# Kernel tuning notes

Hardware: AMD Instinct MI355X
Metric: run time of the kernel (lower is better)

Reference implementation:

```python
import jax, jax.numpy as jnp
import numpy as np

N, H, E, K = 256, 128, 64, 4  # nodes, hidden, dist-embed dim, heads
ALPHA = 0.2  # leaky-relu slope


def setup_inputs() -> dict:
    key = jax.random.key(0)
    ks = jax.random.split(key, 12)
    s = lambda k, sh: (jax.random.normal(k, sh, jnp.float32) * 0.05)
    return dict(
        action_hidden_state=jax.random.normal(ks[0], (N, H), jnp.float32),
        goal_hidden_state=jax.random.normal(ks[1], (N, H), jnp.float32),
        goal=jax.random.normal(ks[2], (N, 2), jnp.float32),
        action=jax.random.normal(ks[3], (N, 2), jnp.float32),
        W_emb=s(ks[4], (1, E)), b_emb=jnp.zeros((E,), jnp.float32),
        W_gate=s(ks[5], (2 * E + 2 * H, H)), b_gate=jnp.zeros((H,), jnp.float32),
        W_gat=s(ks[6], (K, H, H)), a_src=s(ks[7], (K, H)), a_dst=s(ks[8], (K, H)),
        gat_bias=jnp.zeros((H,), jnp.float32),
    )


def cal_dist(goal, action):
    # Vectorized, math-faithful (incl. source typos) version of the O(n^2) loop.
    ax, ay = action[:, 0], action[:, 1]
    gx, gy = goal[:, 0], goal[:, 1]
    a1x, a1y = ax[:, None], ay[:, None]   # node i
    a2x, a2y = ax[None, :], ay[None, :]   # node j
    g1x, g1y = gx[:, None], gy[:, None]
    g2x, g2y = gx[None, :], gy[None, :]
    dn = (a1x - a1x) * (g1y - g2y) - (a1y - a2y) * (g1x - g2x)
    cross_a = a1x * a2y - a1y * a2x
    gterm = g1x * g2y - g1x * g2x
    n1 = cross_a * (g1x - g2x) - (a1x - a2x) * gterm
    n2 = cross_a * (g1y - g2y) - (a1y - a2x) * gterm
    safe = jnp.where(dn == 0.0, 1.0, dn)
    p1, p2 = n1 / safe, n2 / safe
    base = jnp.linalg.norm(action - goal, axis=-1)  # [n]
    d1p = jnp.sqrt((a1x - p1) ** 2 + (a1y - p2) ** 2)
    d2p = jnp.sqrt((a2x - p1) ** 2 + (a2y - p2) ** 2)
    cond = (dn != 0.0) & ((a1x - p1) * (p1 - g1x) > 0.0)
    ones = jnp.ones_like(dn)
    d1 = jnp.where(cond, d1p, base[:, None] * ones)
    d2 = jnp.where(cond, d2p, base[None, :] * ones)
    n = d1.shape[0]
    ii = jnp.arange(n)[:, None]
    jj = jnp.arange(n)[None, :]
    # dist[i,j]=d1(i,j) for i<j; dist[j,i]=d2(i,j) i.e. lower triangle = d2.T; diag = |a_i - g_i|
    return jnp.where(ii == jj, base[:, None] * ones, jnp.where(ii < jj, d1, d2.T))


def reference(action_hidden_state, goal_hidden_state, goal, action,
              W_emb, b_emb, W_gate, b_gate, W_gat, a_src, a_dst, gat_bias):
    ha, hg = action_hidden_state, goal_hidden_state
    n, h = ha.shape
    dist = cal_dist(goal, action)                      # [n,n]
    emb = dist[..., None] * W_emb[0] + b_emb           # Linear(1,E) -> [n,n,E]
    # pairwise interaction gate (i != idx branch, computed for all pairs)
    gate_in = jnp.concatenate([
        jnp.broadcast_to(ha[:, None, :], (n, n, h)),
        jnp.broadcast_to(ha[None, :, :], (n, n, h)),
        emb, jnp.swapaxes(emb, 0, 1)], axis=-1)        # [n,n,2H+2E]
    gate = jax.nn.sigmoid(gate_in @ W_gate + b_gate)   # [n,n,H]
    gated = ha[None, :, :] * gate
    # self branch: gates the goal hidden state; action row stays ungated
    emb_d = emb[jnp.arange(n), jnp.arange(n)]          # [n,E]
    gate_self = jax.nn.sigmoid(
        jnp.concatenate([ha, hg, emb_d, emb_d], axis=-1) @ W_gate + b_gate)
    curr_goal = hg * gate_self                         # [n,H]
    eye = jnp.eye(n, dtype=bool)[..., None]
    curr_action = jnp.where(eye, ha[:, None, :], gated)          # [n,n,H]
    gat_in = jnp.concatenate([curr_action, curr_goal[:, None, :]], axis=1)  # [n,n+1,H]
    # multi-head GAT layer (batched over the n query nodes)
    hp = jnp.einsum('bmf,kfo->bkmo', gat_in, W_gat)    # [n,K,m,H]
    attn = (jnp.einsum('bkmo,ko->bkm', hp, a_src)[..., :, None]
            + jnp.einsum('bkmo,ko->bkm', hp, a_dst)[..., None, :])  # [n,K,m,m]
    attn = jax.nn.softmax(jax.nn.leaky_relu(attn, ALPHA), axis=-1)
    out = jnp.einsum('bkij,bkjo->bkio', attn, hp).mean(axis=1) + gat_bias  # [n,m,H]
    out = jax.nn.elu(out)
    idx = jnp.arange(n)
    return out[idx, idx]                               # [n,H]
```

## Files before the change

kernel.cpp:

```cpp
#include <hip/hip_runtime.h>
#include <math.h>

#define N 256
#define H 128
#define E 64
#define K 4
#define M (N + 1)
#define WAVES 16
#define BLOCK 1024

__device__ __forceinline__ float sigm(float x) {
    return __fdividef(1.0f, 1.0f + __expf(-x));
}

__device__ __forceinline__ float wave_sum(float v) {
#pragma unroll
    for (int d = 1; d < 64; d <<= 1) v += __shfl_xor(v, d, 64);
    return v;
}

__device__ __forceinline__ float readlane_f(float v, int l) {
    return __uint_as_float(__builtin_amdgcn_readlane(__float_as_uint(v), l));
}

__device__ __forceinline__ float kbutterfly(float q0, float q1, float q2, float q3,
                                            int lane) {
    const bool b1 = lane & 1;
    const bool b2 = lane & 2;
    float aA = b1 ? q1 : q0, aB = b1 ? q0 : q1;
    aA += __shfl_xor(aB, 1, 64);
    float cA = b1 ? q3 : q2, cB = b1 ? q2 : q3;
    cA += __shfl_xor(cB, 1, 64);
    float eA = b2 ? cA : aA, eB = b2 ? aA : cA;
    eA += __shfl_xor(eB, 2, 64);
#pragma unroll
    for (int d = 4; d < 64; d <<= 1) eA += __shfl_xor(eA, d, 64);
    return eA;
}

__device__ __forceinline__ void pairdist(
    float a1x, float a1y, float a2x, float a2y,
    float g1x, float g1y, float g2x, float g2y,
    float baseR, float baseC, float& d_rc, float& d_cr)
{
    float t  = __fmul_rn(__fsub_rn(a1y, a2y), __fsub_rn(g1x, g2x));
    float dn = -t;
    float ca = __fsub_rn(__fmul_rn(a1x, a2y), __fmul_rn(a1y, a2x));
    float gt = __fsub_rn(__fmul_rn(g1x, g2y), __fmul_rn(g1x, g2x));
    float n1 = __fsub_rn(__fmul_rn(ca, __fsub_rn(g1x, g2x)),
                         __fmul_rn(__fsub_rn(a1x, a2x), gt));
    float n2 = __fsub_rn(__fmul_rn(ca, __fsub_rn(g1y, g2y)),
                         __fmul_rn(__fsub_rn(a1y, a2x), gt));
    float safe = (dn == 0.0f) ? 1.0f : dn;
    float p1 = __fdiv_rn(n1, safe);
    float p2 = __fdiv_rn(n2, safe);
    bool cond = (dn != 0.0f) &&
                (__fmul_rn(__fsub_rn(a1x, p1), __fsub_rn(p1, g1x)) > 0.0f);
    float dx1 = __fsub_rn(a1x, p1), dy1 = __fsub_rn(a1y, p2);
    float d1p = __fsqrt_rn(__fadd_rn(__fmul_rn(dx1, dx1), __fmul_rn(dy1, dy1)));
    float dx2 = __fsub_rn(a2x, p1), dy2 = __fsub_rn(a2y, p2);
    float d2p = __fsqrt_rn(__fadd_rn(__fmul_rn(dx2, dx2), __fmul_rn(dy2, dy2)));
    d_rc = cond ? d1p : baseR;
    d_cr = cond ? d2p : baseC;
}

__global__ __launch_bounds__(BLOCK) void gat_pre(
    const float* __restrict__ ha, const float* __restrict__ hg,
    const float* __restrict__ W_emb, const float* __restrict__ b_emb,
    const float* __restrict__ W_gate, const float* __restrict__ b_gate,
    const float* __restrict__ W_gat, const float* __restrict__ a_src,
    const float* __restrict__ a_dst,
    float* __restrict__ A1, float* __restrict__ A2, float* __restrict__ G2,
    float* __restrict__ u3g, float* __restrict__ u4g, float* __restrict__ ccg,
    float* __restrict__ vsrc, float* __restrict__ vdst)
{
    const int b    = blockIdx.x;
    const int tid  = threadIdx.x;
    const int wid  = tid >> 6;
    const int lane = tid & 63;

    __shared__ float sRed[8][3][H];

    {
        const int f  = tid & (H - 1);
        const int sl = tid >> 7;
        const int g0 = sl * 16;
        float s1 = 0.f, s2 = 0.f, s3 = 0.f;
#pragma unroll
        for (int g = 0; g < 16; ++g) {
            const int gg = g0 + g;
            float w1 = W_gate[gg * H + f];
            float w2 = W_gate[(H + gg) * H + f];
            float av = ha[b * H + gg];
            float gv = hg[b * H + gg];
            s1 += av * w1;
            s2 += av * w2;
            s3 += gv * w2;
        }
        sRed[sl][0][f] = s1;
        sRed[sl][1][f] = s2;
        sRed[sl][2][f] = s3;
    }
    __syncthreads();
    if (tid < H) {
        float r1 = 0.f, r2 = 0.f, r3 = 0.f;
#pragma unroll
        for (int sl = 0; sl < 8; ++sl) {
            r1 += sRed[sl][0][tid];
            r2 += sRed[sl][1][tid];
            r3 += sRed[sl][2][tid];
        }
        A1[b * H + tid] = r1;
        A2[b * H + tid] = r2;
        G2[b * H + tid] = r3;
    }

    if (b < 8) {
        const int k = b >> 1;
        const float2 as = *(const float2*)&a_src[k * H + lane * 2];
        const float2 ad = *(const float2*)&a_dst[k * H + lane * 2];
#pragma unroll
        for (int it = 0; it < 4; ++it) {
            const int pair = b * 64 + wid * 4 + it;
            const int f    = pair & (H - 1);
            const float2 w = *(const float2*)&W_gat[(k * H + f) * H + lane * 2];
            float vs = wave_sum(w.x * as.x + w.y * as.y);
            float vv = wave_sum(w.x * ad.x + w.y * ad.y);
            if (lane == 0) { vsrc[k * H + f] = vs; vdst[k * H + f] = vv; }
        }
    } else if (b == 8) {
        __syncthreads();
        const int f  = tid & (H - 1);
        const int sl = tid >> 7;
        float s3 = 0.f, s4 = 0.f, scc = 0.f;
#pragma unroll
        for (int e0 = 0; e0 < 8; ++e0) {
            const int e = sl * 8 + e0;
            float w3 = W_gate[(2 * H + e) * H + f];
            float w4 = W_gate[(2 * H + E + e) * H + f];
            float we = W_emb[e], be = b_emb[e];
            s3  += we * w3;
            s4  += we * w4;
            scc += be * (w3 + w4);
        }
        sRed[sl][0][f] = s3;
        sRed[sl][1][f] = s4;
        sRed[sl][2][f] = scc;
        __syncthreads();
        if (tid < H) {
            float r3 = 0.f, r4 = 0.f, rc = 0.f;
#pragma unroll
            for (int sl = 0; sl < 8; ++sl) {
                r3 += sRed[sl][0][tid];
                r4 += sRed[sl][1][tid];
                rc += sRed[sl][2][tid];
            }
            u3g[tid] = r3;
            u4g[tid] = r4;
            ccg[tid] = rc + b_gate[tid];
        }
    }
}

__global__ __launch_bounds__(BLOCK) void gat_main(
    const float* __restrict__ ha, const float* __restrict__ hg,
    const float* __restrict__ W_gat, const float* __restrict__ gat_bias,
    const float* __restrict__ A1, const float* __restrict__ A2,
    const float* __restrict__ G2,
    const float* __restrict__ u3a, const float* __restrict__ u4a,
    const float* __restrict__ cca,
    const float* __restrict__ vsrc, const float* __restrict__ vdst,
    const float* __restrict__ goal, const float* __restrict__ action,
    float* __restrict__ out)
{
    const int i    = blockIdx.x;
    const int tid  = threadIdx.x;
    const int wid  = tid >> 6;
    const int lane = tid & 63;
    const int f0   = lane * 2;

    __shared__ float2 sAct[N];
    __shared__ float2 sGoal[N];
    __shared__ float  sBase[N];
    __shared__ float2 sD[M];
    __shared__ float  sW[WAVES][K][H];
    __shared__ float  sL[WAVES][K];
    __shared__ float  sWfin[K][H];
    __shared__ float  sPart[8][H];

    const float2 a1v = *(const float2*)&A1[i * H + f0];
    const float2 haI = *(const float2*)&ha[i * H + f0];
    const float2 hgI = *(const float2*)&hg[i * H + f0];
    const float2 g2v = *(const float2*)&G2[i * H + f0];
    const float2 u3  = *(const float2*)&u3a[f0];
    const float2 u4  = *(const float2*)&u4a[f0];
    const float2 cc  = *(const float2*)&cca[f0];
    const float2 vd0 = *(const float2*)&vdst[0 * H + f0];
    const float2 vd1 = *(const float2*)&vdst[1 * H + f0];
    const float2 vd2 = *(const float2*)&vdst[2 * H + f0];
    const float2 vd3 = *(const float2*)&vdst[3 * H + f0];
    const float2 vs0 = *(const float2*)&vsrc[0 * H + f0];
    const float2 vs1 = *(const float2*)&vsrc[1 * H + f0];
    const float2 vs2 = *(const float2*)&vsrc[2 * H + f0];
    const float2 vs3 = *(const float2*)&vsrc[3 * H + f0];

    for (int t = tid; t < N; t += BLOCK) {
        float2 a = ((const float2*)action)[t];
        float2 g = ((const float2*)goal)[t];
        sAct[t]  = a;
        sGoal[t] = g;
        float dx = __fsub_rn(a.x, g.x), dy = __fsub_rn(a.y, g.y);
        sBase[t] = __fsqrt_rn(__fadd_rn(__fmul_rn(dx, dx), __fmul_rn(dy, dy)));
    }
    __syncthreads();

    if (tid < M) {
        const int j = tid;
        float dij = 0.f, dji = 0.f;
        if (j != i && j != N) {
            const float2 aI = sAct[i], gI = sGoal[i];
            const float2 aJ = sAct[j], gJ = sGoal[j];
            if (i < j)
                pairdist(aI.x, aI.y, aJ.x, aJ.y, gI.x, gI.y, gJ.x, gJ.y,
                         sBase[i], sBase[j], dij, dji);
            else
                pairdist(aJ.x, aJ.y, aI.x, aI.y, gJ.x, gJ.y, gI.x, gI.y,
                         sBase[j], sBase[i], dji, dij);
        }
        sD[j] = make_float2(dij, dji);
    }

    const float scOwn = kbutterfly(haI.x * vs0.x + haI.y * vs0.y,
                                   haI.x * vs1.x + haI.y * vs1.y,
                                   haI.x * vs2.x + haI.y * vs2.y,
                                   haI.x * vs3.x + haI.y * vs3.y, lane);

    const float2 a1cc = make_float2(a1v.x + cc.x, a1v.y + cc.y);
    const float baseI = sBase[i];
    __syncthreads();

    float l_ = 0.f;
    float w00 = 0.f, w01 = 0.f, w02 = 0.f, w03 = 0.f;
    float w10 = 0.f, w11 = 0.f, w12 = 0.f, w13 = 0.f;

#pragma unroll
    for (int t = 0; t < 16; ++t) {
        const int jj = wid + 16 * t;
        const float2 a2 = *(const float2*)&A2[jj * H + f0];
        const float2 hj = *(const float2*)&ha[jj * H + f0];
        const float2 d  = sD[jj];
        float tx = a1cc.x + a2.x + d.x * u3.x + d.y * u4.x;
        float ty = a1cc.y + a2.y + d.x * u3.y + d.y * u4.y;
        float2 g = make_float2(hj.x * sigm(tx), hj.y * sigm(ty));
        if (jj == i) g = haI;

        float q0 = g.x * vd0.x + g.y * vd0.y;
        float q1 = g.x * vd1.x + g.y * vd1.y;
        float q2 = g.x * vd2.x + g.y * vd2.y;
        float q3 = g.x * vd3.x + g.y * vd3.y;
        float e  = kbutterfly(q0, q1, q2, q3, lane);

        float lg = scOwn + e;
        lg = (lg >= 0.f) ? lg : 0.2f * lg;
        const float p = __expf(lg);
        l_ += p;

        const float p0 = readlane_f(p, 0), p1 = readlane_f(p, 1);
        const float p2 = readlane_f(p, 2), p3 = readlane_f(p, 3);
        w00 += p0 * g.x;  w10 += p0 * g.y;
        w01 += p1 * g.x;  w11 += p1 * g.y;
        w02 += p2 * g.x;  w12 += p2 * g.y;
        w03 += p3 * g.x;  w13 += p3 * g.y;
    }

    if (wid == 0) {
        float tx = a1cc.x + g2v.x + baseI * (u3.x + u4.x);
        float ty = a1cc.y + g2v.y + baseI * (u3.y + u4.y);
        float2 g = make_float2(hgI.x * sigm(tx), hgI.y * sigm(ty));

        float q0 = g.x * vd0.x + g.y * vd0.y;
        float q1 = g.x * vd1.x + g.y * vd1.y;
        float q2 = g.x * vd2.x + g.y * vd2.y;
        float q3 = g.x * vd3.x + g.y * vd3.y;
        float e  = kbutterfly(q0, q1, q2, q3, lane);

        float lg = scOwn + e;
        lg = (lg >= 0.f) ? lg : 0.2f * lg;
        const float p = __expf(lg);
        l_ += p;

        const float p0 = readlane_f(p, 0), p1 = readlane_f(p, 1);
        const float p2 = readlane_f(p, 2), p3 = readlane_f(p, 3);
        w00 += p0 * g.x;  w10 += p0 * g.y;
        w01 += p1 * g.x;  w11 += p1 * g.y;
        w02 += p2 * g.x;  w12 += p2 * g.y;
        w03 += p3 * g.x;  w13 += p3 * g.y;
    }

    *(float2*)&sW[wid][0][f0] = make_float2(w00, w10);
    *(float2*)&sW[wid][1][f0] = make_float2(w01, w11);
    *(float2*)&sW[wid][2][f0] = make_float2(w02, w12);
    *(float2*)&sW[wid][3][f0] = make_float2(w03, w13);
    if (lane < K) sL[wid][lane] = l_;
    __syncthreads();

    if (tid < K * H) {
        const int k = tid >> 7;
        const int f = tid & (H - 1);
        float W = 0.f;
#pragma unroll
        for (int w = 0; w < WAVES; ++w) W += sW[w][k][f];
        float L = 0.f;
#pragma unroll
        for (int w = 0; w < WAVES; ++w) L += sL[w][k];
        sWfin[k][f] = W / L;
    }
    __syncthreads();

    {
        const int f = tid & (H - 1);
        const int s = tid >> 7;
        float acc = 0.0f;
#pragma unroll
        for (int k = 0; k < K; ++k) {
            const int g0 = s * 16;
#pragma unroll
            for (int g = 0; g < 16; ++g)
                acc += sWfin[k][g0 + g] * W_gat[(k * H + g0 + g) * H + f];
        }
        sPart[s][f] = acc;
    }
    __syncthreads();

    if (tid < H) {
        float acc = 0.0f;
#pragma unroll
        for (int s = 0; s < 8; ++s) acc += sPart[s][tid];
        float val = 0.25f * acc + gat_bias[tid];
        out[i * H + tid] = (val > 0.0f) ? val : expm1f(val);
    }
}

extern "C" void kernel_launch(void* const* d_in, const int* in_sizes, int n_in,
                              void* d_out, int out_size, void* d_ws, size_t ws_size,
                              hipStream_t stream)
{
    const float* ha       = (const float*)d_in[0];
    const float* hg       = (const float*)d_in[1];
    const float* goal     = (const float*)d_in[2];
    const float* action   = (const float*)d_in[3];
    const float* W_emb    = (const float*)d_in[4];
    const float* b_emb    = (const float*)d_in[5];
    const float* W_gate   = (const float*)d_in[6];
    const float* b_gate   = (const float*)d_in[7];
    const float* W_gat    = (const float*)d_in[8];
    const float* a_src    = (const float*)d_in[9];
    const float* a_dst    = (const float*)d_in[10];
    const float* gat_bias = (const float*)d_in[11];

    float* ws  = (float*)d_ws;
    float* A1  = ws;
    float* A2  = A1 + N * H;
    float* G2  = A2 + N * H;
    float* u3  = G2 + N * H;
    float* u4  = u3 + H;
    float* cc  = u4 + H;
    float* vs  = cc + H;
    float* vd  = vs + K * H;

    hipLaunchKernelGGL(gat_pre, dim3(N), dim3(BLOCK), 0, stream,
                       ha, hg, W_emb, b_emb, W_gate, b_gate,
                       W_gat, a_src, a_dst,
                       A1, A2, G2, u3, u4, cc, vs, vd);

    hipLaunchKernelGGL(gat_main, dim3(N), dim3(BLOCK), 0, stream,
                       ha, hg, W_gat, gat_bias,
                       A1, A2, G2, u3, u4, cc, vs, vd,
                       goal, action, (float*)d_out);
}
```

Baseline: 28.47 us.

## Pack A2 and ha into float4 rows and spread pre-kernel side work across blocks

The pre-kernel now writes A2 interleaved with the action hidden state as one float4 array, so the main loop issues a single 16-byte load per neighbour instead of two 8-byte loads. The vsrc/vdst projections are spread across all 256 blocks, two waves each, and the u3/u4/cc reduction is split over two blocks instead of being serialized in blocks 0-8. This removes the tail imbalance in the pre-kernel and halves the load instruction count in the hot loop. The cost is an extra shared-memory stage and an extra barrier in the pre-kernel.

```diff
diff --git a/kernel.cpp b/kernel.cpp
--- a/kernel.cpp
+++ b/kernel.cpp
@@ -70,9 +70,10 @@
     const float* __restrict__ W_gate, const float* __restrict__ b_gate,
     const float* __restrict__ W_gat, const float* __restrict__ a_src,
     const float* __restrict__ a_dst,
-    float* __restrict__ A1, float* __restrict__ A2, float* __restrict__ G2,
+    float* __restrict__ A1, float* __restrict__ G2,
     float* __restrict__ u3g, float* __restrict__ u4g, float* __restrict__ ccg,
-    float* __restrict__ vsrc, float* __restrict__ vdst)
+    float* __restrict__ vsrc, float* __restrict__ vdst,
+    float4* __restrict__ pk)
 {
     const int b    = blockIdx.x;
     const int tid  = threadIdx.x;
@@ -80,6 +81,8 @@
     const int lane = tid & 63;
 
     __shared__ float sRed[8][3][H];
+    __shared__ float sA2[H];
+    __shared__ float sU[8][3][64];
 
     {
         const int f  = tid & (H - 1);
@@ -101,37 +104,22 @@
         sRed[sl][1][f] = s2;
         sRed[sl][2][f] = s3;
     }
-    __syncthreads();
-    if (tid < H) {
-        float r1 = 0.f, r2 = 0.f, r3 = 0.f;
-#pragma unroll
-        for (int sl = 0; sl < 8; ++sl) {
-            r1 += sRed[sl][0][tid];
-            r2 += sRed[sl][1][tid];
-            r3 += sRed[sl][2][tid];
-        }
-        A1[b * H + tid] = r1;
-        A2[b * H + tid] = r2;
-        G2[b * H + tid] = r3;
-    }
-
-    if (b < 8) {
-        const int k = b >> 1;
-        const float2 as = *(const float2*)&a_src[k * H + lane * 2];
-        const float2 ad = *(const float2*)&a_dst[k * H + lane * 2];
-#pragma unroll
-        for (int it = 0; it < 4; ++it) {
-            const int pair = b * 64 + wid * 4 + it;
-            const int f    = pair & (H - 1);
-            const float2 w = *(const float2*)&W_gat[(k * H + f) * H + lane * 2];
-            float vs = wave_sum(w.x * as.x + w.y * as.y);
-            float vv = wave_sum(w.x * ad.x + w.y * ad.y);
-            if (lane == 0) { vsrc[k * H + f] = vs; vdst[k * H + f] = vv; }
-        }
-    } else if (b == 8) {
-        __syncthreads();
-        const int f  = tid & (H - 1);
-        const int sl = tid >> 7;
+
+    if (wid >= 14) {
+        const int p = 2 * b + (wid - 14);
+        const int k = p >> 7;
+        const int f = p & (H - 1);
+        const float2 w2 = ((const float2*)&W_gat[(k * H + f) * H])[lane];
+        const float2 as2 = ((const float2*)&a_src[k * H])[lane];
+        const float2 ad2 = ((const float2*)&a_dst[k * H])[lane];
+        float vsv = wave_sum(w2.x * as2.x + w2.y * as2.y);
+        float vdv = wave_sum(w2.x * ad2.x + w2.y * ad2.y);
+        if (lane == 0) { vsrc[k * H + f] = vsv; vdst[k * H + f] = vdv; }
+    }
+
+    if (b < 2 && wid >= 2 && wid < 10) {
+        const int sl = wid - 2;
+        const int f  = (b << 6) | lane;
         float s3 = 0.f, s4 = 0.f, scc = 0.f;
 #pragma unroll
         for (int e0 = 0; e0 < 8; ++e0) {
@@ -143,33 +131,51 @@
             s4  += we * w4;
             scc += be * (w3 + w4);
         }
-        sRed[sl][0][f] = s3;
-        sRed[sl][1][f] = s4;
-        sRed[sl][2][f] = scc;
-        __syncthreads();
-        if (tid < H) {
-            float r3 = 0.f, r4 = 0.f, rc = 0.f;
-#pragma unroll
-            for (int sl = 0; sl < 8; ++sl) {
-                r3 += sRed[sl][0][tid];
-                r4 += sRed[sl][1][tid];
-                rc += sRed[sl][2][tid];
-            }
-            u3g[tid] = r3;
-            u4g[tid] = r4;
-            ccg[tid] = rc + b_gate[tid];
-        }
+        sU[sl][0][lane] = s3;
+        sU[sl][1][lane] = s4;
+        sU[sl][2][lane] = scc;
+    }
+    __syncthreads();
+
+    if (tid < H) {
+        float r1 = 0.f, r2 = 0.f, r3 = 0.f;
+#pragma unroll
+        for (int sl = 0; sl < 8; ++sl) {
+            r1 += sRed[sl][0][tid];
+            r2 += sRed[sl][1][tid];
+            r3 += sRed[sl][2][tid];
+        }
+        A1[b * H + tid] = r1;
+        G2[b * H + tid] = r3;
+        sA2[tid] = r2;
+    }
+    __syncthreads();
+
+    if (tid < 64) {
+        const float2 h2 = ((const float2*)&ha[b * H])[tid];
+        pk[(b << 6) | tid] = make_float4(sA2[2 * tid], sA2[2 * tid + 1], h2.x, h2.y);
+    }
+    if (b < 2 && tid < 192) {
+        const int c  = tid >> 6;
+        const int fl = tid & 63;
+        float r = 0.f;
+#pragma unroll
+        for (int w = 0; w < 8; ++w) r += sU[w][c][fl];
+        const int f = (b << 6) | fl;
+        if (c == 0)      u3g[f] = r;
+        else if (c == 1) u4g[f] = r;
+        else             ccg[f] = r + b_gate[f];
     }
 }
 
 __global__ __launch_bounds__(BLOCK) void gat_main(
     const float* __restrict__ ha, const float* __restrict__ hg,
     const float* __restrict__ W_gat, const float* __restrict__ gat_bias,
-    const float* __restrict__ A1, const float* __restrict__ A2,
-    const float* __restrict__ G2,
+    const float* __restrict__ A1, const float* __restrict__ G2,
     const float* __restrict__ u3a, const float* __restrict__ u4a,
     const float* __restrict__ cca,
     const float* __restrict__ vsrc, const float* __restrict__ vdst,
+    const float4* __restrict__ pk,
     const float* __restrict__ goal, const float* __restrict__ action,
     float* __restrict__ out)
 {
@@ -204,13 +210,13 @@
     const float2 vs2 = *(const float2*)&vsrc[2 * H + f0];
     const float2 vs3 = *(const float2*)&vsrc[3 * H + f0];
 
-    for (int t = tid; t < N; t += BLOCK) {
-        float2 a = ((const float2*)action)[t];
-        float2 g = ((const float2*)goal)[t];
-        sAct[t]  = a;
-        sGoal[t] = g;
+    if (tid < N) {
+        float2 a = ((const float2*)action)[tid];
+        float2 g = ((const float2*)goal)[tid];
+        sAct[tid]  = a;
+        sGoal[tid] = g;
         float dx = __fsub_rn(a.x, g.x), dy = __fsub_rn(a.y, g.y);
-        sBase[t] = __fsqrt_rn(__fadd_rn(__fmul_rn(dx, dx), __fmul_rn(dy, dy)));
+        sBase[tid] = __fsqrt_rn(__fadd_rn(__fmul_rn(dx, dx), __fmul_rn(dy, dy)));
     }
     __syncthreads();
 
@@ -246,12 +252,11 @@
 #pragma unroll
     for (int t = 0; t < 16; ++t) {
         const int jj = wid + 16 * t;
-        const float2 a2 = *(const float2*)&A2[jj * H + f0];
-        const float2 hj = *(const float2*)&ha[jj * H + f0];
+        const float4 ph = pk[(jj << 6) | lane];
         const float2 d  = sD[jj];
-        float tx = a1cc.x + a2.x + d.x * u3.x + d.y * u4.x;
-        float ty = a1cc.y + a2.y + d.x * u3.y + d.y * u4.y;
-        float2 g = make_float2(hj.x * sigm(tx), hj.y * sigm(ty));
+        float tx = a1cc.x + ph.x + d.x * u3.x + d.y * u4.x;
+        float ty = a1cc.y + ph.y + d.x * u3.y + d.y * u4.y;
+        float2 g = make_float2(ph.z * sigm(tx), ph.w * sigm(ty));
         if (jj == i) g = haI;
 
         float q0 = g.x * vd0.x + g.y * vd0.y;
@@ -359,22 +364,22 @@
     const float* gat_bias = (const float*)d_in[11];
 
     float* ws  = (float*)d_ws;
-    float* A1  = ws;
-    float* A2  = A1 + N * H;
-    float* G2  = A2 + N * H;
-    float* u3  = G2 + N * H;
-    float* u4  = u3 + H;
-    float* cc  = u4 + H;
-    float* vs  = cc + H;
-    float* vd  = vs + K * H;
+    float*  A1 = ws;
+    float*  G2 = A1 + N * H;
+    float*  u3 = G2 + N * H;
+    float*  u4 = u3 + H;
+    float*  cc = u4 + H;
+    float*  vs = cc + H;
+    float*  vd = vs + K * H;
+    float4* pk = (float4*)(vd + K * H);
 
     hipLaunchKernelGGL(gat_pre, dim3(N), dim3(BLOCK), 0, stream,
                        ha, hg, W_emb, b_emb, W_gate, b_gate,
                        W_gat, a_src, a_dst,
-                       A1, A2, G2, u3, u4, cc, vs, vd);
+                       A1, G2, u3, u4, cc, vs, vd, pk);
 
     hipLaunchKernelGGL(gat_main, dim3(N), dim3(BLOCK), 0, stream,
                        ha, hg, W_gat, gat_bias,
-                       A1, A2, G2, u3, u4, cc, vs, vd,
+                       A1, G2, u3, u4, cc, vs, vd, pk,
                        goal, action, (float*)d_out);
 }
```

Result: faster. 26.50 us (-6.9%).
